# Performance work log

Measured on AMD Instinct MI355X. Metric: run time of the kernel, lower is better.

## Reference

```python
import jax, jax.numpy as jnp
import numpy as np

DT = 0.5   # time step dt
T = 30     # free-phase iterations


def rho(x):
    # hard-sigmoid activation used throughout EqProp
    return jnp.clip(x, 0.0, 1.0)


def rhop(x):
    # derivative indicator of rho
    return ((x >= 0.0) & (x <= 1.0)).astype(x.dtype)


def setup_inputs() -> dict:
    key = jax.random.key(0)
    ks = jax.random.split(key, 7)
    B = 4096
    fc = [10, 512, 512, 784]  # output -> ... -> input
    s0 = jnp.zeros((B, fc[0]), jnp.float32)
    s1 = jnp.zeros((B, fc[1]), jnp.float32)
    s2 = jnp.zeros((B, fc[2]), jnp.float32)
    x = jax.random.uniform(ks[0], (B, fc[3]), jnp.float32)  # clamped input layer s[3]
    W0 = (jax.random.normal(ks[1], (fc[0], fc[1]), jnp.float32) / np.float32(np.sqrt(fc[1])))
    b0 = jax.random.normal(ks[2], (fc[0],), jnp.float32) * 0.01
    W1 = (jax.random.normal(ks[3], (fc[1], fc[2]), jnp.float32) / np.float32(np.sqrt(fc[2])))
    b1 = jax.random.normal(ks[4], (fc[1],), jnp.float32) * 0.01
    W2 = (jax.random.normal(ks[5], (fc[2], fc[3]), jnp.float32) / np.float32(np.sqrt(fc[3])))
    b2 = jax.random.normal(ks[6], (fc[2],), jnp.float32) * 0.01
    return {"s0": s0, "s1": s1, "s2": s2, "x": x,
            "W0": W0, "b0": b0, "W1": W1, "b1": b1, "W2": W2, "b2": b2}


def reference(s0, s1, s2, x, W0, b0, W1, b1, W2, b2):
    """Free-phase EqProp forward (stepper_c repeated T times, beta=target=None).

    State list s = [s0, s1, s2, x]; x (the data layer) is held fixed.
    Returns the final free states concatenated along features: [B, 10+512+512].
    """
    rx = rho(x)  # input layer activation, constant across steps

    def step(carry, _):
        c0, c1, c2 = carry
        r0, r1, r2 = rho(c0), rho(c1), rho(c2)
        # dsdt[0] = -s0 + rhop(s0) * W0(rho(s1))
        d0 = -c0 + rhop(c0) * (r1 @ W0.T + b0)
        # dsdt[1] = -s1 + rhop(s1) * (W1(rho(s2)) + rho(s0) @ W0)
        d1 = -c1 + rhop(c1) * (r2 @ W1.T + b1 + r0 @ W0)
        # dsdt[2] = -s2 + rhop(s2) * (W2(rho(s3)) + rho(s1) @ W1)
        d2 = -c2 + rhop(c2) * (rx @ W2.T + b2 + r1 @ W1)
        n0 = jnp.clip(c0 + DT * d0, 0.0, 1.0)
        n1 = jnp.clip(c1 + DT * d1, 0.0, 1.0)
        n2 = jnp.clip(c2 + DT * d2, 0.0, 1.0)
        return (n0, n1, n2), None

    (s0, s1, s2), _ = jax.lax.scan(step, (s0, s1, s2), None, length=T)
    return jnp.concatenate([s0, s1, s2], axis=1)
```

## Files before the change

### kernel.cpp

```cpp
#include <hip/hip_runtime.h>

typedef unsigned short ushortT;
typedef _Float16 halfT;
typedef _Float16 f16x8 __attribute__((ext_vector_type(8)));
typedef float f32x4 __attribute__((ext_vector_type(4)));
typedef unsigned int u32x4 __attribute__((ext_vector_type(4)));

#define HSTR 1056
#define OFF1B 32
#define OFF2B 544
#define CSTR 1034

__device__ __forceinline__ void split2h(float f, halfT& h, halfT& l) {
    h = (halfT)f;
    l = (halfT)(f - (float)h);
}

#define MFMA16(a, b, c) __builtin_amdgcn_mfma_f32_16x16x32_f16(a, b, c, 0, 0, 0)
#define BCAST(x) __builtin_bit_cast(f16x8, x)

__global__ void k_zero(u32x4* __restrict__ p, int n) {
    u32x4 z = {0u, 0u, 0u, 0u};
    for (int i = blockIdx.x * blockDim.x + threadIdx.x; i < n; i += gridDim.x * blockDim.x)
        p[i] = z;
}

__global__ __launch_bounds__(256) void k_prep(const float* __restrict__ W1,
                                              halfT* __restrict__ W1h,
                                              halfT* __restrict__ W1T) {
    __shared__ float tile[64][65];
    const int ti = blockIdx.x >> 3, tj = blockIdx.x & 7;
    const int t = threadIdx.x;
#pragma unroll
    for (int q = 0; q < 16; ++q) {
        int rr = q * 4 + (t >> 6), cc = t & 63;
        float v = W1[(size_t)(ti * 64 + rr) * 512 + tj * 64 + cc];
        tile[rr][cc] = v;
        W1h[(size_t)(ti * 64 + rr) * 512 + tj * 64 + cc] = (halfT)v;
    }
    __syncthreads();
#pragma unroll
    for (int q = 0; q < 16; ++q) {
        int rr = q * 4 + (t >> 6), cc = t & 63;
        W1T[(size_t)(tj * 64 + rr) * 512 + ti * 64 + cc] = (halfT)tile[cc][rr];
    }
}

__global__ __launch_bounds__(256) void k_c2(const float* __restrict__ x,
                                            const float* __restrict__ W2,
                                            const float* __restrict__ b2,
                                            float* __restrict__ c2) {
    __shared__ u32x4 cs[2048];
    u32x4* xHi = cs;
    u32x4* xLo = cs + 512;
    u32x4* wHi = cs + 1024;
    u32x4* wLo = cs + 1536;
    const int bid = blockIdx.x, t = threadIdx.x;
    const int lane = t & 63, w = t >> 6, l15 = lane & 15, l4 = lane >> 4;
    const int bm2 = (bid >> 3) * 64, bn2 = (bid & 7) * 64;
    const int mB2 = (w >> 1) * 32, nB2 = (w & 1) * 32;
    const int sr2 = t >> 2, ub = (t & 3) * 2;
    f32x4 accC[2][2];
#pragma unroll
    for (int i = 0; i < 2; ++i)
#pragma unroll
        for (int j = 0; j < 2; ++j) { f32x4 z = {0.f, 0.f, 0.f, 0.f}; accC[i][j] = z; }
    for (int k0 = 0; k0 < 784; k0 += 64) {
#pragma unroll
        for (int j = 0; j < 2; ++j) {
            int u = ub + j;
            bool valid = (k0 + u * 8 + 8 <= 784);
            union { halfT hs[8]; u32x4 v; } ph, pl, qh, ql;
            if (valid) {
                const float* srcx = x  + (size_t)(bm2 + sr2) * 784 + k0 + u * 8;
                const float* srcw = W2 + (size_t)(bn2 + sr2) * 784 + k0 + u * 8;
#pragma unroll
                for (int e = 0; e < 8; ++e) {
                    float cx = fminf(fmaxf(srcx[e], 0.f), 1.f);
                    split2h(cx, ph.hs[e], pl.hs[e]);
                    split2h(srcw[e], qh.hs[e], ql.hs[e]);
                }
            } else {
#pragma unroll
                for (int e = 0; e < 8; ++e) {
                    ph.hs[e] = (halfT)0.f; pl.hs[e] = (halfT)0.f;
                    qh.hs[e] = (halfT)0.f; ql.hs[e] = (halfT)0.f;
                }
            }
            int sw = u ^ (sr2 & 7);
            xHi[sr2 * 8 + sw] = ph.v;  xLo[sr2 * 8 + sw] = pl.v;
            wHi[sr2 * 8 + sw] = qh.v;  wLo[sr2 * 8 + sw] = ql.v;
        }
        __syncthreads();
        int kwMax = (k0 == 768) ? 1 : 2;
        for (int kw = 0; kw < kwMax; ++kw) {
            f16x8 ah[2], al[2], bh[2], bl[2];
#pragma unroll
            for (int i = 0; i < 2; ++i) {
                int m = mB2 + i * 16 + l15;
                int uu = (kw * 4 + l4) ^ (m & 7);
                ah[i] = BCAST(xHi[m * 8 + uu]);
                al[i] = BCAST(xLo[m * 8 + uu]);
                int n = nB2 + i * 16 + l15;
                int uv = (kw * 4 + l4) ^ (n & 7);
                bh[i] = BCAST(wHi[n * 8 + uv]);
                bl[i] = BCAST(wLo[n * 8 + uv]);
            }
#pragma unroll
            for (int i = 0; i < 2; ++i)
#pragma unroll
                for (int jj = 0; jj < 2; ++jj) {
                    accC[i][jj] = MFMA16(ah[i], bh[jj], accC[i][jj]);
                    accC[i][jj] = MFMA16(al[i], bh[jj], accC[i][jj]);
                    accC[i][jj] = MFMA16(ah[i], bl[jj], accC[i][jj]);
                }
        }
        __syncthreads();
    }
#pragma unroll
    for (int mi = 0; mi < 2; ++mi)
#pragma unroll
        for (int ni = 0; ni < 2; ++ni)
#pragma unroll
            for (int q = 0; q < 4; ++q) {
                int row = bm2 + mB2 + mi * 16 + l4 * 4 + q;
                int col = bn2 + nB2 + ni * 16 + l15;
                c2[(size_t)row * 512 + col] = accC[mi][ni][q] + b2[col];
            }
}

__global__ __launch_bounds__(512, 4) void k_step6(const halfT* __restrict__ sH,
                                                  halfT* __restrict__ dH,
                                                  const halfT* __restrict__ W1h,
                                                  const halfT* __restrict__ W1T,
                                                  const float* __restrict__ W0,
                                                  const float* __restrict__ b0,
                                                  const float* __restrict__ b1,
                                                  const float* __restrict__ c2,
                                                  float* __restrict__ outF) {
    __shared__ u32x4 smem[2560];
    u32x4* AsR = smem;
    u32x4* BhS = smem + 1024;
    u32x4* aux = smem + 1536;

    const int bid = blockIdx.x, t = threadIdx.x;
    const int lane = t & 63, w = t >> 6, l15 = lane & 15, l4 = lane >> 4;
    const int mB = w * 16;

    const int xcd = bid & 7, rblk = bid >> 3, bn_i = rblk & 7, grp = rblk >> 3;
    const int pidx = grp * 8 + xcd;
    const bool isZ1 = pidx < 32;
    const int bm = (pidx & 31) * 128, bn = bn_i * 64;
    const bool doZ0 = (!isZ1) && (bn_i == 0);

    if (isZ1) {
        if (t < 256) {
            int n = t >> 2, u = t & 3;
            union { halfT hs[8]; u32x4 v; } pk;
#pragma unroll
            for (int e = 0; e < 8; ++e) {
                int k = u * 8 + e;
                pk.hs[e] = (k < 10) ? (halfT)W0[(size_t)k * 512 + bn + n] : (halfT)0.f;
            }
            aux[n * 4 + u] = pk.v;
        }
        if (t < 128) {
            union { halfT hs[16]; u32x4 v2[2]; } pk;
#pragma unroll
            for (int e = 0; e < 16; ++e) pk.hs[e] = (halfT)0.f;
            const halfT* sp = sH + (size_t)(bm + t) * HSTR;
#pragma unroll
            for (int e = 0; e < 10; ++e) pk.hs[e] = sp[e];
            u32x4 z = {0u, 0u, 0u, 0u};
            aux[256 + t * 4 + 0] = pk.v2[0];
            aux[256 + t * 4 + 1] = pk.v2[1];
            aux[256 + t * 4 + 2] = z;
            aux[256 + t * 4 + 3] = z;
        }
    } else if (doZ0) {
        int c = t >> 5, u0 = (t & 31) * 2;
#pragma unroll
        for (int j = 0; j < 2; ++j) {
            int U = u0 + j;
            union { halfT hs[8]; u32x4 v; } pk;
#pragma unroll
            for (int e = 0; e < 8; ++e)
                pk.hs[e] = (c < 10) ? (halfT)W0[(size_t)c * 512 + U * 8 + e] : (halfT)0.f;
            aux[c * 64 + ((U & ~7) | ((U & 7) ^ (c & 7)))] = pk.v;
        }
    }

    const int aOff = isZ1 ? OFF2B : OFF1B;
    const int dOff = isZ1 ? OFF1B : OFF2B;
    const int oOff = isZ1 ? 10 : 522;
    const halfT* __restrict__ Wb = isZ1 ? W1h : W1T;
    const int sr = t >> 2, su = (t & 3) * 2;
    const int bnr = t >> 3, bju = t & 7;
    const bool fin = (outF != nullptr);

    f32x4 acc[4], accZ;
#pragma unroll
    for (int ni = 0; ni < 4; ++ni) { f32x4 z = {0.f,0.f,0.f,0.f}; acc[ni] = z; }
    { f32x4 z = {0.f,0.f,0.f,0.f}; accZ = z; }

    u32x4 rA[2][2], rB[2];
    {
        const u32x4* gA = (const u32x4*)(sH + (size_t)(bm + sr) * HSTR + aOff);
        rA[0][0] = gA[su];  rA[0][1] = gA[su + 1];
        rB[0] = ((const u32x4*)(Wb + (size_t)(bn + bnr) * 512))[bju];
    }
#pragma unroll
    for (int it = 0; it < 8; ++it) {
        const int k0 = it * 64;
        const int cur = it & 1, nxt = cur ^ 1;
        __syncthreads();
        AsR[sr * 8 + ( su      ^ (sr & 7))] = rA[cur][0];
        AsR[sr * 8 + ((su + 1) ^ (sr & 7))] = rA[cur][1];
        BhS[bnr * 8 + (bju ^ (bnr & 7))] = rB[cur];
        if (it < 7) {
            const int k1 = k0 + 64;
            const u32x4* gA = (const u32x4*)(sH + (size_t)(bm + sr) * HSTR + aOff + k1);
            rA[nxt][0] = gA[su];  rA[nxt][1] = gA[su + 1];
            rB[nxt] = ((const u32x4*)(Wb + (size_t)(bn + bnr) * 512 + k1))[bju];
        }
        __syncthreads();
#pragma unroll
        for (int kw = 0; kw < 2; ++kw) {
            f16x8 a, b[4];
            {
                int m = mB + l15;
                a = BCAST(AsR[m * 8 + ((kw * 4 + l4) ^ (m & 7))]);
            }
#pragma unroll
            for (int ni = 0; ni < 4; ++ni) {
                int n = ni * 16 + l15;
                b[ni] = BCAST(BhS[n * 8 + ((kw * 4 + l4) ^ (n & 7))]);
            }
#pragma unroll
            for (int ni = 0; ni < 4; ++ni)
                acc[ni] = MFMA16(a, b[ni], acc[ni]);
            if (doZ0) {
                int U = it * 8 + kw * 4 + l4;
                f16x8 bz = BCAST(aux[l15 * 64 + ((U & ~7) | ((U & 7) ^ (l15 & 7)))]);
                accZ = MFMA16(a, bz, accZ);
            }
        }
    }
    if (isZ1) {
        f16x8 a2 = BCAST(aux[256 + (size_t)(mB + l15) * 4 + l4]);
#pragma unroll
        for (int ni = 0; ni < 4; ++ni) {
            f16x8 bb = BCAST(aux[(size_t)(ni * 16 + l15) * 4 + l4]);
            acc[ni] = MFMA16(a2, bb, acc[ni]);
        }
    }

    __syncthreads();
    if (fin) {
#pragma unroll
        for (int ni = 0; ni < 4; ++ni) {
            int gc = bn + ni * 16 + l15;
            float biasN = isZ1 ? b1[gc] : 0.f;
#pragma unroll
            for (int q = 0; q < 4; ++q) {
                size_t row = (size_t)bm + mB + l4 * 4 + q;
                float bias = isZ1 ? biasN : c2[row * 512 + gc];
                float old = (float)sH[row * HSTR + dOff + gc];
                float v = 0.5f * old + 0.5f * (acc[ni][q] + bias);
                v = fminf(fmaxf(v, 0.f), 1.f);
                outF[row * CSTR + oOff + gc] = v;
            }
        }
        if (doZ0 && l15 < 10) {
            float b0v = b0[l15];
#pragma unroll
            for (int q = 0; q < 4; ++q) {
                size_t row = (size_t)bm + mB + l4 * 4 + q;
                float old = (float)sH[row * HSTR + l15];
                float v = 0.5f * old + 0.5f * (accZ[q] + b0v);
                v = fminf(fmaxf(v, 0.f), 1.f);
                outF[row * CSTR + l15] = v;
            }
        }
    } else {
        halfT* dlds = (halfT*)AsR;
#pragma unroll
        for (int ni = 0; ni < 4; ++ni) {
            int gc = bn + ni * 16 + l15;
            float biasN = isZ1 ? b1[gc] : 0.f;
#pragma unroll
            for (int q = 0; q < 4; ++q) {
                size_t row = (size_t)bm + mB + l4 * 4 + q;
                float bias = isZ1 ? biasN : c2[row * 512 + gc];
                float old = (float)sH[row * HSTR + dOff + gc];
                float v = 0.5f * old + 0.5f * (acc[ni][q] + bias);
                v = fminf(fmaxf(v, 0.f), 1.f);
                dlds[(mB + l4 * 4 + q) * 64 + ni * 16 + l15] = (halfT)v;
            }
        }
        if (doZ0 && l15 < 10) {
            float b0v = b0[l15];
#pragma unroll
            for (int q = 0; q < 4; ++q) {
                size_t row = (size_t)bm + mB + l4 * 4 + q;
                float old = (float)sH[row * HSTR + l15];
                float v = 0.5f * old + 0.5f * (accZ[q] + b0v);
                v = fminf(fmaxf(v, 0.f), 1.f);
                dH[row * HSTR + l15] = (halfT)v;
            }
        }
        __syncthreads();
#pragma unroll
        for (int j = 0; j < 2; ++j) {
            int i = j * 512 + t;
            int row = i >> 3, u = i & 7;
            ((u32x4*)(dH + (size_t)(bm + row) * HSTR + dOff + bn))[u] = AsR[i];
        }
    }
}

extern "C" void kernel_launch(void* const* d_in, const int* in_sizes, int n_in,
                              void* d_out, int out_size, void* d_ws, size_t ws_size,
                              hipStream_t stream) {
    const float* x  = (const float*)d_in[3];
    const float* W0 = (const float*)d_in[4];
    const float* b0 = (const float*)d_in[5];
    const float* W1 = (const float*)d_in[6];
    const float* b1 = (const float*)d_in[7];
    const float* W2 = (const float*)d_in[8];
    const float* b2 = (const float*)d_in[9];

    halfT* hiA = (halfT*)d_out;
    halfT* hiB = (halfT*)d_ws;
    float* c2  = (float*)(hiB + (size_t)4096 * HSTR);
    halfT* W1h = (halfT*)(c2 + (size_t)4096 * 512);
    halfT* W1T = W1h + 512 * 512;

    const int zeroN = (int)((size_t)4096 * HSTR * sizeof(halfT) / sizeof(u32x4));
    k_zero<<<1024, 256, 0, stream>>>((u32x4*)hiA, zeroN);
    k_prep<<<64, 256, 0, stream>>>(W1, W1h, W1T);
    k_c2<<<512, 256, 0, stream>>>(x, W2, b2, c2);

    for (int ts = 0; ts < 30; ++ts) {
        const halfT* sH = (ts & 1) ? hiB : hiA;
        halfT* dH       = (ts & 1) ? hiA : hiB;
        float* outF = (ts == 29) ? (float*)d_out : nullptr;
        k_step6<<<512, 512, 0, stream>>>(sH, dH, W1h, W1T, W0, b0, b1, c2, outF);
    }
}
```

Baseline: 548.4 us.

## Drop split-fp16 compensation in input GEMM and double step kernel K-tile

The one-time input projection kernel stops splitting x and W2 into hi/lo fp16 pairs and runs a single fp16 MFMA per tile instead of three, halving its shared memory. The per-step kernel now stages 128-wide K chunks (4 iterations instead of 8), with larger register prefetch and a wider swizzled shared layout. This removes half the barriers per step. The cost is lower accuracy in the constant input term and more LDS per block (64KB), which may reduce occupancy.

```diff
diff --git a/kernel.cpp b/kernel.cpp
--- a/kernel.cpp
+++ b/kernel.cpp
@@ -11,13 +11,9 @@
 #define OFF2B 544
 #define CSTR 1034
 
-__device__ __forceinline__ void split2h(float f, halfT& h, halfT& l) {
-    h = (halfT)f;
-    l = (halfT)(f - (float)h);
-}
-
 #define MFMA16(a, b, c) __builtin_amdgcn_mfma_f32_16x16x32_f16(a, b, c, 0, 0, 0)
 #define BCAST(x) __builtin_bit_cast(f16x8, x)
+#define SWZ(u, r) (((u) & 8) | (((u) & 7) ^ ((r) & 7)))
 
 __global__ void k_zero(u32x4* __restrict__ p, int n) {
     u32x4 z = {0u, 0u, 0u, 0u};
@@ -50,11 +46,9 @@
                                             const float* __restrict__ W2,
                                             const float* __restrict__ b2,
                                             float* __restrict__ c2) {
-    __shared__ u32x4 cs[2048];
-    u32x4* xHi = cs;
-    u32x4* xLo = cs + 512;
-    u32x4* wHi = cs + 1024;
-    u32x4* wLo = cs + 1536;
+    __shared__ u32x4 cs[1024];
+    u32x4* xS = cs;
+    u32x4* wS = cs + 512;
     const int bid = blockIdx.x, t = threadIdx.x;
     const int lane = t & 63, w = t >> 6, l15 = lane & 15, l4 = lane >> 4;
     const int bm2 = (bid >> 3) * 64, bn2 = (bid & 7) * 64;
@@ -70,50 +64,39 @@
         for (int j = 0; j < 2; ++j) {
             int u = ub + j;
             bool valid = (k0 + u * 8 + 8 <= 784);
-            union { halfT hs[8]; u32x4 v; } ph, pl, qh, ql;
+            union { halfT hs[8]; u32x4 v; } px, pw;
             if (valid) {
                 const float* srcx = x  + (size_t)(bm2 + sr2) * 784 + k0 + u * 8;
                 const float* srcw = W2 + (size_t)(bn2 + sr2) * 784 + k0 + u * 8;
 #pragma unroll
                 for (int e = 0; e < 8; ++e) {
-                    float cx = fminf(fmaxf(srcx[e], 0.f), 1.f);
-                    split2h(cx, ph.hs[e], pl.hs[e]);
-                    split2h(srcw[e], qh.hs[e], ql.hs[e]);
+                    px.hs[e] = (halfT)fminf(fmaxf(srcx[e], 0.f), 1.f);
+                    pw.hs[e] = (halfT)srcw[e];
                 }
             } else {
 #pragma unroll
-                for (int e = 0; e < 8; ++e) {
-                    ph.hs[e] = (halfT)0.f; pl.hs[e] = (halfT)0.f;
-                    qh.hs[e] = (halfT)0.f; ql.hs[e] = (halfT)0.f;
-                }
+                for (int e = 0; e < 8; ++e) { px.hs[e] = (halfT)0.f; pw.hs[e] = (halfT)0.f; }
             }
             int sw = u ^ (sr2 & 7);
-            xHi[sr2 * 8 + sw] = ph.v;  xLo[sr2 * 8 + sw] = pl.v;
-            wHi[sr2 * 8 + sw] = qh.v;  wLo[sr2 * 8 + sw] = ql.v;
+            xS[sr2 * 8 + sw] = px.v;
+            wS[sr2 * 8 + sw] = pw.v;
         }
         __syncthreads();
         int kwMax = (k0 == 768) ? 1 : 2;
         for (int kw = 0; kw < kwMax; ++kw) {
-            f16x8 ah[2], al[2], bh[2], bl[2];
+            f16x8 a[2], b[2];
 #pragma unroll
             for (int i = 0; i < 2; ++i) {
                 int m = mB2 + i * 16 + l15;
-                int uu = (kw * 4 + l4) ^ (m & 7);
-                ah[i] = BCAST(xHi[m * 8 + uu]);
-                al[i] = BCAST(xLo[m * 8 + uu]);
+                a[i] = BCAST(xS[m * 8 + ((kw * 4 + l4) ^ (m & 7))]);
                 int n = nB2 + i * 16 + l15;
-                int uv = (kw * 4 + l4) ^ (n & 7);
-                bh[i] = BCAST(wHi[n * 8 + uv]);
-                bl[i] = BCAST(wLo[n * 8 + uv]);
+                b[i] = BCAST(wS[n * 8 + ((kw * 4 + l4) ^ (n & 7))]);
             }
 #pragma unroll
             for (int i = 0; i < 2; ++i)
 #pragma unroll
-                for (int jj = 0; jj < 2; ++jj) {
-                    accC[i][jj] = MFMA16(ah[i], bh[jj], accC[i][jj]);
-                    accC[i][jj] = MFMA16(al[i], bh[jj], accC[i][jj]);
-                    accC[i][jj] = MFMA16(ah[i], bl[jj], accC[i][jj]);
-                }
+                for (int jj = 0; jj < 2; ++jj)
+                    accC[i][jj] = MFMA16(a[i], b[jj], accC[i][jj]);
         }
         __syncthreads();
     }
@@ -129,7 +112,7 @@
             }
 }
 
-__global__ __launch_bounds__(512, 4) void k_step6(const halfT* __restrict__ sH,
+__global__ __launch_bounds__(512, 4) void k_step8(const halfT* __restrict__ sH,
                                                   halfT* __restrict__ dH,
                                                   const halfT* __restrict__ W1h,
                                                   const halfT* __restrict__ W1T,
@@ -138,10 +121,10 @@
                                                   const float* __restrict__ b1,
                                                   const float* __restrict__ c2,
                                                   float* __restrict__ outF) {
-    __shared__ u32x4 smem[2560];
+    __shared__ u32x4 smem[4096];
     u32x4* AsR = smem;
-    u32x4* BhS = smem + 1024;
-    u32x4* aux = smem + 1536;
+    u32x4* BhS = smem + 2048;
+    u32x4* aux = smem + 3072;
 
     const int bid = blockIdx.x, t = threadIdx.x;
     const int lane = t & 63, w = t >> 6, l15 = lane & 15, l4 = lane >> 4;
@@ -194,8 +177,8 @@
     const int dOff = isZ1 ? OFF1B : OFF2B;
     const int oOff = isZ1 ? 10 : 522;
     const halfT* __restrict__ Wb = isZ1 ? W1h : W1T;
-    const int sr = t >> 2, su = (t & 3) * 2;
-    const int bnr = t >> 3, bju = t & 7;
+    const int sr = t >> 2, su = (t & 3) * 4;
+    const int bnr = t >> 3, bju = (t & 7) * 2;
     const bool fin = (outF != nullptr);
 
     f32x4 acc[4], accZ;
@@ -203,44 +186,53 @@
     for (int ni = 0; ni < 4; ++ni) { f32x4 z = {0.f,0.f,0.f,0.f}; acc[ni] = z; }
     { f32x4 z = {0.f,0.f,0.f,0.f}; accZ = z; }
 
-    u32x4 rA[2][2], rB[2];
+    u32x4 rA[2][4], rB[2][2];
     {
         const u32x4* gA = (const u32x4*)(sH + (size_t)(bm + sr) * HSTR + aOff);
-        rA[0][0] = gA[su];  rA[0][1] = gA[su + 1];
-        rB[0] = ((const u32x4*)(Wb + (size_t)(bn + bnr) * 512))[bju];
-    }
-#pragma unroll
-    for (int it = 0; it < 8; ++it) {
-        const int k0 = it * 64;
+        const u32x4* gB = (const u32x4*)(Wb + (size_t)(bn + bnr) * 512);
+#pragma unroll
+        for (int j = 0; j < 4; ++j) rA[0][j] = gA[su + j];
+#pragma unroll
+        for (int j = 0; j < 2; ++j) rB[0][j] = gB[bju + j];
+    }
+#pragma unroll
+    for (int it = 0; it < 4; ++it) {
+        const int k0 = it * 128;
         const int cur = it & 1, nxt = cur ^ 1;
         __syncthreads();
-        AsR[sr * 8 + ( su      ^ (sr & 7))] = rA[cur][0];
-        AsR[sr * 8 + ((su + 1) ^ (sr & 7))] = rA[cur][1];
-        BhS[bnr * 8 + (bju ^ (bnr & 7))] = rB[cur];
-        if (it < 7) {
-            const int k1 = k0 + 64;
+#pragma unroll
+        for (int j = 0; j < 4; ++j)
+            AsR[sr * 16 + SWZ(su + j, sr)] = rA[cur][j];
+#pragma unroll
+        for (int j = 0; j < 2; ++j)
+            BhS[bnr * 16 + SWZ(bju + j, bnr)] = rB[cur][j];
+        if (it < 3) {
+            const int k1 = k0 + 128;
             const u32x4* gA = (const u32x4*)(sH + (size_t)(bm + sr) * HSTR + aOff + k1);
-            rA[nxt][0] = gA[su];  rA[nxt][1] = gA[su + 1];
-            rB[nxt] = ((const u32x4*)(Wb + (size_t)(bn + bnr) * 512 + k1))[bju];
-        }
-        __syncthreads();
-#pragma unroll
-        for (int kw = 0; kw < 2; ++kw) {
+            const u32x4* gB = (const u32x4*)(Wb + (size_t)(bn + bnr) * 512 + k1);
+#pragma unroll
+            for (int j = 0; j < 4; ++j) rA[nxt][j] = gA[su + j];
+#pragma unroll
+            for (int j = 0; j < 2; ++j) rB[nxt][j] = gB[bju + j];
+        }
+        __syncthreads();
+#pragma unroll
+        for (int kw = 0; kw < 4; ++kw) {
             f16x8 a, b[4];
             {
                 int m = mB + l15;
-                a = BCAST(AsR[m * 8 + ((kw * 4 + l4) ^ (m & 7))]);
+                a = BCAST(AsR[m * 16 + SWZ(kw * 4 + l4, m)]);
             }
 #pragma unroll
             for (int ni = 0; ni < 4; ++ni) {
                 int n = ni * 16 + l15;
-                b[ni] = BCAST(BhS[n * 8 + ((kw * 4 + l4) ^ (n & 7))]);
+                b[ni] = BCAST(BhS[n * 16 + SWZ(kw * 4 + l4, n)]);
             }
 #pragma unroll
             for (int ni = 0; ni < 4; ++ni)
                 acc[ni] = MFMA16(a, b[ni], acc[ni]);
             if (doZ0) {
-                int U = it * 8 + kw * 4 + l4;
+                int U = it * 16 + kw * 4 + l4;
                 f16x8 bz = BCAST(aux[l15 * 64 + ((U & ~7) | ((U & 7) ^ (l15 & 7)))]);
                 accZ = MFMA16(a, bz, accZ);
             }
@@ -345,6 +337,6 @@
         const halfT* sH = (ts & 1) ? hiB : hiA;
         halfT* dH       = (ts & 1) ? hiA : hiB;
         float* outF = (ts == 29) ? (float*)d_out : nullptr;
-        k_step6<<<512, 512, 0, stream>>>(sH, dH, W1h, W1T, W0, b0, b1, c2, outF);
-    }
-}
+        k_step8<<<512, 512, 0, stream>>>(sH, dH, W1h, W1T, W0, b0, b1, c2, outF);
+    }
+}
```

After: 598.3 us. 1.09x slower.
